# Kernel optimization log

Hardware: AMD Instinct MI355X
Metric: run time of the kernel (lower is better)

The kernel has to match this reference:

```python
import jax, jax.numpy as jnp
import numpy as np

TAU = 0.07
EPS = 1e-12  # matches torch F.normalize default eps


def setup_inputs() -> dict:
    key = jax.random.key(0)
    k1, k2 = jax.random.split(key)
    B, C, H, W, K = 4, 256, 256, 256, 19
    feat = jax.random.normal(k1, (B, C, H, W), dtype=jnp.float32)
    # binary ground-truth one-hot-ish masks; gt.eq(1) selects positives
    gt = jax.random.randint(k2, (B, K, H, W), 0, 2).astype(jnp.float32)
    return {"feat": feat, "gt": gt}


def _l2norm(x, axis):
    n = jnp.sqrt(jnp.sum(x * x, axis=axis, keepdims=True))
    return x / jnp.maximum(n, EPS)


def reference(feat, gt):
    # feat: [B,C,H,W], gt: [B,K,H,W] binary
    pos = (gt == 1.0).astype(feat.dtype)              # [B,K,H,W]
    fnorm = _l2norm(feat, axis=1)                     # per-pixel L2 normalize over C
    # scatter-add normalized features into class prototypes
    k0 = jnp.einsum('bkhw,bchw->kc', pos, fnorm)      # [K,C]
    k0n = _l2norm(k0, axis=1)                         # [K,C]
    # prototype-vs-pixel similarities, softmax over classes
    logits = jnp.einsum('kc,bchw->bkhw', k0n, fnorm) / TAU  # [B,K,H,W]
    logp = jax.nn.log_softmax(logits, axis=1)
    num_pos = jnp.sum(pos)
    loss = -jnp.sum(pos * logp) / num_pos
    return loss
```

## Files before the change

kernel.cpp:

```cpp
#include <hip/hip_runtime.h>
#include <math.h>

namespace {
constexpr int Bn = 4;
constexpr int Cn = 256;
constexpr int Kn = 19;
constexpr int HW = 256 * 256;
constexpr int P  = Bn * HW;
constexpr float TAUv = 0.07f;
constexpr float EPSv = 1e-12f;

constexpr int K0_OFF   = 0;
constexpr int K0N_OFF  = 4864;
constexpr int SUMS_OFF = 9728;
constexpr int P1_GRID  = 512;
constexpr int ZERO_N   = 9730;
}

__global__ __launch_bounds__(256) void gc_init(float* __restrict__ ws) {
  int i = blockIdx.x * 256 + threadIdx.x;
  if (i < ZERO_N) ws[i] = 0.0f;
}

__global__ __launch_bounds__(256, 2) void gc_phase1(const float* __restrict__ feat,
                                                    const float* __restrict__ gt,
                                                    float* __restrict__ k0) {
  __shared__ float tile[64 * 256];
  __shared__ float part[256];
  __shared__ float2 pm[64];

  const int t    = threadIdx.x;
  const int lane = t & 63;
  const int wv   = t >> 6;

  float acc[Kn];
#pragma unroll
  for (int k = 0; k < Kn; k++) acc[k] = 0.0f;

  for (int tid = blockIdx.x; tid < P / 64; tid += gridDim.x) {
    const int p0  = tid << 6;
    const int b   = p0 >> 16;
    const int hw0 = p0 & (HW - 1);
    const float* fb = feat + (size_t)b * (Cn * HW) + hw0 + lane;

    __syncthreads();

    float ss = 0.0f;
#pragma unroll 8
    for (int j = 0; j < 64; j++) {
      const int c = (wv << 6) + j;
      const float v = fb[(size_t)c * HW];
      ss += v * v;
      tile[(lane << 8) + (c ^ (lane & 31))] = v;
    }
    part[t] = ss;

    unsigned my_mask = 0;
    if (wv == 0) {
      const float* gb = gt + (size_t)b * (Kn * HW) + hw0 + lane;
#pragma unroll
      for (int k = 0; k < Kn; k++)
        my_mask |= (gb[(size_t)k * HW] == 1.0f) ? (1u << k) : 0u;
    }

    __syncthreads();

    if (wv == 0) {
      const float fss = part[lane] + part[64 + lane] + part[128 + lane] + part[192 + lane];
      const float rn = 1.0f / fmaxf(sqrtf(fss), EPSv);
      pm[lane] = make_float2(rn, __uint_as_float(my_mask));
    }

    __syncthreads();

#pragma unroll 4
    for (int p = 0; p < 64; p++) {
      const float2 pr = pm[p];
      const float rp = __uint_as_float(__builtin_amdgcn_readfirstlane(__float_as_uint(pr.x)));
      const unsigned m = __builtin_amdgcn_readfirstlane(__float_as_uint(pr.y));
      const float fv = tile[(p << 8) + (t ^ (p & 31))] * rp;
#pragma unroll
      for (int k = 0; k < Kn; k++) {
        const float w = (float)((m >> k) & 1u);
        acc[k] = fmaf(fv, w, acc[k]);
      }
    }
  }

#pragma unroll
  for (int k = 0; k < Kn; k++) atomicAdd(&k0[k * 256 + t], acc[k]);
}

__global__ __launch_bounds__(256) void gc_phase2(const float* __restrict__ k0,
                                                 float* __restrict__ k0n) {
  const int lane = threadIdx.x & 63;
  const int wv   = threadIdx.x >> 6;
  for (int r = wv; r < Kn; r += 4) {
    float s = 0.0f;
#pragma unroll
    for (int j = 0; j < 4; j++) {
      const float v = k0[r * 256 + (j << 6) + lane];
      s += v * v;
    }
#pragma unroll
    for (int off = 32; off > 0; off >>= 1) s += __shfl_down(s, off);
    s = __shfl(s, 0);
    const float rn = 1.0f / fmaxf(sqrtf(s), EPSv);
#pragma unroll
    for (int j = 0; j < 4; j++) {
      const int c = (j << 6) + lane;
      k0n[r * 256 + c] = k0[r * 256 + c] * rn;
    }
  }
}

__global__ __launch_bounds__(256) void gc_phase3(const float* __restrict__ feat,
                                                 const float* __restrict__ gt,
                                                 const float* __restrict__ k0n,
                                                 float* __restrict__ sums) {
  const int t   = threadIdx.x;
  const int pix = (blockIdx.x << 8) + t;
  const int b   = pix >> 16;
  const int hw  = pix & (HW - 1);
  const float* fb = feat + (size_t)b * (Cn * HW) + hw;

  float dot[Kn];
#pragma unroll
  for (int k = 0; k < Kn; k++) dot[k] = 0.0f;
  float ss = 0.0f;

  for (int c0 = 0; c0 < Cn; c0 += 16) {
    float f[16];
#pragma unroll
    for (int j = 0; j < 16; j++) f[j] = fb[(size_t)(c0 + j) * HW];
#pragma unroll
    for (int j = 0; j < 16; j++) ss = fmaf(f[j], f[j], ss);
#pragma unroll
    for (int k = 0; k < Kn; k++) {
      const float* row = k0n + k * 256 + c0;
      float d = dot[k];
#pragma unroll
      for (int j = 0; j < 16; j++) d = fmaf(f[j], row[j], d);
      dot[k] = d;
    }
  }

  const float sc = 1.0f / (fmaxf(sqrtf(ss), EPSv) * TAUv);
  float mx = -1e30f;
#pragma unroll
  for (int k = 0; k < Kn; k++) { dot[k] *= sc; mx = fmaxf(mx, dot[k]); }
  float se = 0.0f;
#pragma unroll
  for (int k = 0; k < Kn; k++) se += __expf(dot[k] - mx);
  const float lse = __logf(se) + mx;

  const float* gb = gt + (size_t)b * (Kn * HW) + hw;
  float lsum = 0.0f;
  float npos = 0.0f;
#pragma unroll
  for (int k = 0; k < Kn; k++) {
    if (gb[(size_t)k * HW] == 1.0f) { lsum += lse - dot[k]; npos += 1.0f; }
  }

#pragma unroll
  for (int off = 32; off > 0; off >>= 1) {
    lsum += __shfl_down(lsum, off);
    npos += __shfl_down(npos, off);
  }
  if ((t & 63) == 0) {
    atomicAdd(&sums[0], lsum);
    atomicAdd(&sums[1], npos);
  }
}

__global__ void gc_finalize(const float* __restrict__ sums, float* __restrict__ out) {
  if (threadIdx.x == 0 && blockIdx.x == 0)
    out[0] = sums[0] / sums[1];
}

extern "C" void kernel_launch(void* const* d_in, const int* in_sizes, int n_in,
                              void* d_out, int out_size, void* d_ws, size_t ws_size,
                              hipStream_t stream) {
  const float* feat = (const float*)d_in[0];
  const float* gt   = (const float*)d_in[1];
  float* ws  = (float*)d_ws;
  float* out = (float*)d_out;

  float* k0   = ws + K0_OFF;
  float* k0n  = ws + K0N_OFF;
  float* sums = ws + SUMS_OFF;

  gc_init<<<dim3((ZERO_N + 255) / 256), dim3(256), 0, stream>>>(ws);
  gc_phase1<<<dim3(P1_GRID), dim3(256), 0, stream>>>(feat, gt, k0);
  gc_phase2<<<dim3(1), dim3(256), 0, stream>>>(k0, k0n);
  gc_phase3<<<dim3(P / 256), dim3(256), 0, stream>>>(feat, gt, k0n, sums);
  gc_finalize<<<dim3(1), dim3(64), 0, stream>>>(sums, out);
}
```

Measured before the change: 652.8 us.

## Restructure both reduction passes with smaller tiles, LDS weights, and prefetch

Phase 1 now uses 32-pixel tiles with 8 groups of 32 channels, and loads all 32 channel values into registers before storing them to LDS. It precomputes per-pixel masked weights (the mask bit times the inverse norm) in shared memory, so the inner loop reads float4 weights instead of decoding bitmasks. It also doubles the grid and raises the occupancy hint to 4. Phase 3 stages the normalized prototypes in LDS and reads them as float4, and it software-prefetches the next 16-channel chunk of features through an LDS tile. These changes target global/scalar load latency and ALU work in the inner loops, at the cost of extra LDS traffic and barriers per chunk.

```diff
diff --git a/kernel.cpp b/kernel.cpp
--- a/kernel.cpp
+++ b/kernel.cpp
@@ -2,19 +2,19 @@
 #include <math.h>
 
 namespace {
-constexpr int Bn = 4;
 constexpr int Cn = 256;
 constexpr int Kn = 19;
 constexpr int HW = 256 * 256;
-constexpr int P  = Bn * HW;
+constexpr int P  = 4 * HW;
 constexpr float TAUv = 0.07f;
 constexpr float EPSv = 1e-12f;
 
 constexpr int K0_OFF   = 0;
 constexpr int K0N_OFF  = 4864;
 constexpr int SUMS_OFF = 9728;
-constexpr int P1_GRID  = 512;
 constexpr int ZERO_N   = 9730;
+constexpr int P1_GRID  = 1024;
+constexpr int P3_GRID  = P / 256;
 }
 
 __global__ __launch_bounds__(256) void gc_init(float* __restrict__ ws) {
@@ -22,68 +22,81 @@
   if (i < ZERO_N) ws[i] = 0.0f;
 }
 
-__global__ __launch_bounds__(256, 2) void gc_phase1(const float* __restrict__ feat,
+__global__ __launch_bounds__(256, 4) void gc_phase1(const float* __restrict__ feat,
                                                     const float* __restrict__ gt,
                                                     float* __restrict__ k0) {
-  __shared__ float tile[64 * 256];
+  __shared__ float tile[32 * 256];
   __shared__ float part[256];
-  __shared__ float2 pm[64];
-
-  const int t    = threadIdx.x;
-  const int lane = t & 63;
-  const int wv   = t >> 6;
+  __shared__ float wls[32][20];
+
+  const int t = threadIdx.x;
+  const int p = t & 31;
+  const int g = t >> 5;
 
   float acc[Kn];
 #pragma unroll
   for (int k = 0; k < Kn; k++) acc[k] = 0.0f;
 
-  for (int tid = blockIdx.x; tid < P / 64; tid += gridDim.x) {
-    const int p0  = tid << 6;
+  for (int tid = blockIdx.x; tid < P / 32; tid += gridDim.x) {
+    const int p0  = tid << 5;
     const int b   = p0 >> 16;
     const int hw0 = p0 & (HW - 1);
-    const float* fb = feat + (size_t)b * (Cn * HW) + hw0 + lane;
-
-    __syncthreads();
-
+    const float* fb = feat + (size_t)b * (Cn * HW) + hw0;
+
+    __syncthreads();
+
+    float v[32];
+#pragma unroll
+    for (int j = 0; j < 32; j++) v[j] = fb[(size_t)((g << 5) + j) * HW + p];
     float ss = 0.0f;
-#pragma unroll 8
-    for (int j = 0; j < 64; j++) {
-      const int c = (wv << 6) + j;
-      const float v = fb[(size_t)c * HW];
-      ss += v * v;
-      tile[(lane << 8) + (c ^ (lane & 31))] = v;
+#pragma unroll
+    for (int j = 0; j < 32; j++) {
+      const int c = (g << 5) + j;
+      ss += v[j] * v[j];
+      tile[(p << 8) + (c ^ p)] = v[j];
     }
     part[t] = ss;
 
-    unsigned my_mask = 0;
-    if (wv == 0) {
-      const float* gb = gt + (size_t)b * (Kn * HW) + hw0 + lane;
+    unsigned msk = 0;
+    if (t < 32) {
+      const float* gb = gt + (size_t)b * (Kn * HW) + hw0 + p;
 #pragma unroll
       for (int k = 0; k < Kn; k++)
-        my_mask |= (gb[(size_t)k * HW] == 1.0f) ? (1u << k) : 0u;
-    }
-
-    __syncthreads();
-
-    if (wv == 0) {
-      const float fss = part[lane] + part[64 + lane] + part[128 + lane] + part[192 + lane];
+        msk |= (gb[(size_t)k * HW] == 1.0f) ? (1u << k) : 0u;
+    }
+
+    __syncthreads();
+
+    if (t < 32) {
+      float fss = 0.0f;
+#pragma unroll
+      for (int q = 0; q < 8; q++) fss += part[(q << 5) + p];
       const float rn = 1.0f / fmaxf(sqrtf(fss), EPSv);
-      pm[lane] = make_float2(rn, __uint_as_float(my_mask));
+#pragma unroll
+      for (int k = 0; k < Kn; k++) wls[p][k] = ((msk >> k) & 1u) ? rn : 0.0f;
+      wls[p][19] = 0.0f;
     }
 
     __syncthreads();
 
 #pragma unroll 4
-    for (int p = 0; p < 64; p++) {
-      const float2 pr = pm[p];
-      const float rp = __uint_as_float(__builtin_amdgcn_readfirstlane(__float_as_uint(pr.x)));
-      const unsigned m = __builtin_amdgcn_readfirstlane(__float_as_uint(pr.y));
-      const float fv = tile[(p << 8) + (t ^ (p & 31))] * rp;
-#pragma unroll
-      for (int k = 0; k < Kn; k++) {
-        const float w = (float)((m >> k) & 1u);
-        acc[k] = fmaf(fv, w, acc[k]);
-      }
+    for (int pp = 0; pp < 32; pp++) {
+      const float4 w0 = *(const float4*)&wls[pp][0];
+      const float4 w1 = *(const float4*)&wls[pp][4];
+      const float4 w2 = *(const float4*)&wls[pp][8];
+      const float4 w3 = *(const float4*)&wls[pp][12];
+      const float4 w4 = *(const float4*)&wls[pp][16];
+      const float fv = tile[(pp << 8) + (t ^ pp)];
+      acc[0]  = fmaf(fv, w0.x, acc[0]);  acc[1]  = fmaf(fv, w0.y, acc[1]);
+      acc[2]  = fmaf(fv, w0.z, acc[2]);  acc[3]  = fmaf(fv, w0.w, acc[3]);
+      acc[4]  = fmaf(fv, w1.x, acc[4]);  acc[5]  = fmaf(fv, w1.y, acc[5]);
+      acc[6]  = fmaf(fv, w1.z, acc[6]);  acc[7]  = fmaf(fv, w1.w, acc[7]);
+      acc[8]  = fmaf(fv, w2.x, acc[8]);  acc[9]  = fmaf(fv, w2.y, acc[9]);
+      acc[10] = fmaf(fv, w2.z, acc[10]); acc[11] = fmaf(fv, w2.w, acc[11]);
+      acc[12] = fmaf(fv, w3.x, acc[12]); acc[13] = fmaf(fv, w3.y, acc[13]);
+      acc[14] = fmaf(fv, w3.z, acc[14]); acc[15] = fmaf(fv, w3.w, acc[15]);
+      acc[16] = fmaf(fv, w4.x, acc[16]); acc[17] = fmaf(fv, w4.y, acc[17]);
+      acc[18] = fmaf(fv, w4.z, acc[18]);
     }
   }
 
@@ -114,14 +127,20 @@
   }
 }
 
-__global__ __launch_bounds__(256) void gc_phase3(const float* __restrict__ feat,
-                                                 const float* __restrict__ gt,
-                                                 const float* __restrict__ k0n,
-                                                 float* __restrict__ sums) {
-  const int t   = threadIdx.x;
-  const int pix = (blockIdx.x << 8) + t;
-  const int b   = pix >> 16;
-  const int hw  = pix & (HW - 1);
+__global__ __launch_bounds__(256, 4) void gc_phase3(const float* __restrict__ feat,
+                                                    const float* __restrict__ gt,
+                                                    const float* __restrict__ k0n,
+                                                    float* __restrict__ sums) {
+  __shared__ float wco[Kn * 256];
+  __shared__ float tile[16 * 256];
+
+  const int t = threadIdx.x;
+#pragma unroll
+  for (int i = 0; i < Kn; i++) wco[i * 256 + t] = k0n[i * 256 + t];
+
+  const int pix0 = blockIdx.x << 8;
+  const int b    = pix0 >> 16;
+  const int hw   = (pix0 & (HW - 1)) + t;
   const float* fb = feat + (size_t)b * (Cn * HW) + hw;
 
   float dot[Kn];
@@ -129,19 +148,34 @@
   for (int k = 0; k < Kn; k++) dot[k] = 0.0f;
   float ss = 0.0f;
 
+  float v[16];
+#pragma unroll
+  for (int j = 0; j < 16; j++) v[j] = fb[(size_t)j * HW];
+
   for (int c0 = 0; c0 < Cn; c0 += 16) {
-    float f[16];
-#pragma unroll
-    for (int j = 0; j < 16; j++) f[j] = fb[(size_t)(c0 + j) * HW];
-#pragma unroll
-    for (int j = 0; j < 16; j++) ss = fmaf(f[j], f[j], ss);
-#pragma unroll
-    for (int k = 0; k < Kn; k++) {
-      const float* row = k0n + k * 256 + c0;
-      float d = dot[k];
-#pragma unroll
-      for (int j = 0; j < 16; j++) d = fmaf(f[j], row[j], d);
-      dot[k] = d;
+    __syncthreads();
+#pragma unroll
+    for (int j = 0; j < 16; j++) tile[j * 256 + t] = v[j];
+    __syncthreads();
+
+    if (c0 + 16 < Cn) {
+#pragma unroll
+      for (int j = 0; j < 16; j++) v[j] = fb[(size_t)(c0 + 16 + j) * HW];
+    }
+
+#pragma unroll
+    for (int j4 = 0; j4 < 16; j4 += 4) {
+      const float f0 = tile[(j4 + 0) * 256 + t];
+      const float f1 = tile[(j4 + 1) * 256 + t];
+      const float f2 = tile[(j4 + 2) * 256 + t];
+      const float f3 = tile[(j4 + 3) * 256 + t];
+      ss = fmaf(f0, f0, ss); ss = fmaf(f1, f1, ss);
+      ss = fmaf(f2, f2, ss); ss = fmaf(f3, f3, ss);
+#pragma unroll
+      for (int k = 0; k < Kn; k++) {
+        const float4 w = *(const float4*)&wco[k * 256 + c0 + j4];
+        dot[k] = fmaf(f3, w.w, fmaf(f2, w.z, fmaf(f1, w.y, fmaf(f0, w.x, dot[k]))));
+      }
     }
   }
 
@@ -155,8 +189,7 @@
   const float lse = __logf(se) + mx;
 
   const float* gb = gt + (size_t)b * (Kn * HW) + hw;
-  float lsum = 0.0f;
-  float npos = 0.0f;
+  float lsum = 0.0f, npos = 0.0f;
 #pragma unroll
   for (int k = 0; k < Kn; k++) {
     if (gb[(size_t)k * HW] == 1.0f) { lsum += lse - dot[k]; npos += 1.0f; }
@@ -193,6 +226,6 @@
   gc_init<<<dim3((ZERO_N + 255) / 256), dim3(256), 0, stream>>>(ws);
   gc_phase1<<<dim3(P1_GRID), dim3(256), 0, stream>>>(feat, gt, k0);
   gc_phase2<<<dim3(1), dim3(256), 0, stream>>>(k0, k0n);
-  gc_phase3<<<dim3(P / 256), dim3(256), 0, stream>>>(feat, gt, k0n, sums);
+  gc_phase3<<<dim3(P3_GRID), dim3(256), 0, stream>>>(feat, gt, k0n, sums);
   gc_finalize<<<dim3(1), dim3(64), 0, stream>>>(sums, out);
 }
```

Result: faster. 602.0 us (-7.8%).
